# Optimization experiments

Measured on AMD Instinct MI355X. Metric: run time of the kernel, lower is better.

The kernel has to match this reference:

```python
import jax, jax.numpy as jnp
import numpy as np

B, S, D = 2, 2048, 1024
H = 16
HD = D // H  # head_dim = 64


def setup_inputs() -> dict:
    key = jax.random.key(0)
    ks = jax.random.split(key, 9)
    std = 1.0 / np.sqrt(HD)
    inp = {
        "X": jax.random.normal(ks[0], (B, S, D), dtype=jnp.float32),
        # per-head Q/K/V Linear weights stacked: [H, head_dim, head_dim], biases [H, head_dim]
        "Wq": jax.random.uniform(ks[1], (H, HD, HD), jnp.float32, -std, std),
        "bq": jax.random.uniform(ks[2], (H, HD), jnp.float32, -std, std),
        "Wk": jax.random.uniform(ks[3], (H, HD, HD), jnp.float32, -std, std),
        "bk": jax.random.uniform(ks[4], (H, HD), jnp.float32, -std, std),
        "Wv": jax.random.uniform(ks[5], (H, HD, HD), jnp.float32, -std, std),
        "bv": jax.random.uniform(ks[6], (H, HD), jnp.float32, -std, std),
        # output projection: [D, D] (in, out layout), bias [D]
        "Wo": jax.random.uniform(ks[7], (D, D), jnp.float32, -1.0 / np.sqrt(D), 1.0 / np.sqrt(D)),
        "bo": jax.random.uniform(ks[8], (D,), jnp.float32, -1.0 / np.sqrt(D), 1.0 / np.sqrt(D)),
    }
    return inp


def reference(X, Wq, bq, Wk, bk, Wv, bv, Wo, bo):
    # Split hidden dim into heads: [B, S, H, HD]
    x = X.reshape(B, S, H, HD)
    scale = jnp.sqrt(jnp.asarray(HD, dtype=X.dtype))
    # Per-head linear projections (batched over heads)
    Q = jnp.einsum("bshd,hde->bshe", x, Wq) + bq
    K = jnp.einsum("bshd,hde->bshe", x, Wk) + bk
    V = jnp.einsum("bshd,hde->bshe", x, Wv) + bv
    # Attention scores [B, H, S, S]
    scores = jnp.einsum("bshd,bthd->bhst", Q, K) / scale
    attn = jax.nn.softmax(scores, axis=-1)
    # Weighted values -> [B, S, H, HD] -> concat -> [B, S, D]
    out = jnp.einsum("bhst,bthd->bshd", attn, V).reshape(B, S, D)
    return out @ Wo + bo
```

## Files before the change

### kernel.cpp

```cpp
#include <hip/hip_runtime.h>
#include <stdint.h>

#define B_  2
#define S_  2048
#define D_  1024
#define H_  16
#define HD_ 64
#define TOK (B_*S_)

typedef __bf16 bf16x8 __attribute__((ext_vector_type(8)));
typedef __bf16 bf16x4 __attribute__((ext_vector_type(4)));
typedef float  f32x4  __attribute__((ext_vector_type(4)));

static_assert(sizeof(bf16x8) == 16, "bf16x8 must be 16B");
static_assert(sizeof(bf16x4) == 8,  "bf16x4 must be 8B");

__device__ __forceinline__ float fexp2(float x) { return __builtin_amdgcn_exp2f(x); }

__device__ __forceinline__ f32x4 mfma16(bf16x8 a, bf16x8 b, f32x4 c) {
    return __builtin_amdgcn_mfma_f32_16x16x32_bf16(a, b, c, 0, 0, 0);
}

__global__ __launch_bounds__(256) void k_transpose_wo(
    const float* __restrict__ Wo, unsigned short* __restrict__ WoT)
{
    __shared__ float t[64][65];
    const int i0 = blockIdx.x * 64;
    const int o0 = blockIdx.y * 64;
    const int tid = threadIdx.x;
    #pragma unroll
    for (int p = 0; p < 16; ++p) {
        int idx = tid + p * 256;
        int r = idx >> 6, c = idx & 63;
        t[r][c] = Wo[(size_t)(i0 + r) * D_ + o0 + c];
    }
    __syncthreads();
    #pragma unroll
    for (int p = 0; p < 16; ++p) {
        int idx = tid + p * 256;
        int r = idx >> 6, c = idx & 63;
        reinterpret_cast<__bf16*>(WoT)[(size_t)(o0 + r) * D_ + i0 + c] = (__bf16)t[c][r];
    }
}

__global__ __launch_bounds__(256) void k_qkv(
    const float* __restrict__ X,
    const float* __restrict__ Wq, const float* __restrict__ bq,
    const float* __restrict__ Wk, const float* __restrict__ bk,
    const float* __restrict__ Wv, const float* __restrict__ bv,
    unsigned short* __restrict__ Qo, unsigned short* __restrict__ Ko,
    unsigned short* __restrict__ Vt)
{
    __shared__ float          Wf[64][65];
    __shared__ unsigned short Xl[128 * 64];
    __shared__ unsigned short Wl[64 * 64];

    const int tid  = threadIdx.x;
    const int lane = tid & 63, w = tid >> 6;
    const int g = lane >> 4, q = lane & 15;
    const int tok0 = blockIdx.x * 128;
    const int h    = blockIdx.y;
    const int z    = blockIdx.z;
    const float* W  = (z == 0) ? Wq : (z == 1) ? Wk : Wv;
    const float* bb = (z == 0) ? bq : (z == 1) ? bk : bv;

    #pragma unroll
    for (int i = 0; i < 4; ++i) {
        int c = tid + 256 * i;
        int r = c >> 4, c4 = (c & 15) * 4;
        *reinterpret_cast<float4*>(&Wf[r][c4]) =
            *reinterpret_cast<const float4*>(&W[h * 4096 + r * 64 + c4]);
    }
    #pragma unroll
    for (int i = 0; i < 4; ++i) {
        int c = tid + 256 * i;
        int row = c >> 3, slot = c & 7;
        const float* src = &X[(size_t)(tok0 + row) * D_ + h * HD_ + slot * 8];
        float4 x0 = *reinterpret_cast<const float4*>(src);
        float4 x1 = *reinterpret_cast<const float4*>(src + 4);
        bf16x8 v = { (__bf16)x0.x, (__bf16)x0.y, (__bf16)x0.z, (__bf16)x0.w,
                     (__bf16)x1.x, (__bf16)x1.y, (__bf16)x1.z, (__bf16)x1.w };
        *reinterpret_cast<bf16x8*>(
            reinterpret_cast<char*>(Xl) + row * 128 + ((slot ^ (row & 7)) * 16)) = v;
    }
    __syncthreads();

    #pragma unroll
    for (int i = 0; i < 2; ++i) {
        int c = tid + 256 * i;
        int e = c >> 3, slot = c & 7;
        bf16x8 v;
        #pragma unroll
        for (int j = 0; j < 8; ++j) v[j] = (__bf16)Wf[slot * 8 + j][e];
        *reinterpret_cast<bf16x8*>(
            reinterpret_cast<char*>(Wl) + e * 128 + ((slot ^ (e & 7)) * 16)) = v;
    }
    __syncthreads();

    f32x4 acc[2][4] = {};
    #pragma unroll
    for (int s = 0; s < 2; ++s) {
        bf16x8 af[2], bfr[4];
        #pragma unroll
        for (int am = 0; am < 2; ++am) {
            int row  = w * 32 + am * 16 + q;
            int slot = (s * 4 + g) ^ (row & 7);
            af[am] = *reinterpret_cast<const bf16x8*>(
                reinterpret_cast<const char*>(Xl) + row * 128 + slot * 16);
        }
        #pragma unroll
        for (int bn = 0; bn < 4; ++bn) {
            int row  = bn * 16 + q;
            int slot = (s * 4 + g) ^ (row & 7);
            bfr[bn] = *reinterpret_cast<const bf16x8*>(
                reinterpret_cast<const char*>(Wl) + row * 128 + slot * 16);
        }
        #pragma unroll
        for (int am = 0; am < 2; ++am)
            #pragma unroll
            for (int bn = 0; bn < 4; ++bn)
                acc[am][bn] = mfma16(af[am], bfr[bn], acc[am][bn]);
    }

    const float scq = 0.18033688011112042f;
    const int b  = tok0 >> 11;
    const int sb = (tok0 & (S_ - 1)) + w * 32;
    #pragma unroll
    for (int bn = 0; bn < 4; ++bn) {
        int e = bn * 16 + q;
        float bia = bb[h * HD_ + e];
        #pragma unroll
        for (int am = 0; am < 2; ++am) {
            int s4 = sb + am * 16 + 4 * g;
            if (z == 2) {
                bf16x4 ov = { (__bf16)(acc[am][bn][0] + bia), (__bf16)(acc[am][bn][1] + bia),
                              (__bf16)(acc[am][bn][2] + bia), (__bf16)(acc[am][bn][3] + bia) };
                *reinterpret_cast<bf16x4*>(
                    &Vt[((size_t)(b * H_ + h) * HD_ + e) * S_ + s4]) = ov;
            } else {
                float sc = (z == 0) ? scq : 1.0f;
                unsigned short* dst = (z == 0) ? Qo : Ko;
                __bf16* d16 = reinterpret_cast<__bf16*>(dst);
                #pragma unroll
                for (int j = 0; j < 4; ++j)
                    d16[((size_t)(b * H_ + h) * S_ + s4 + j) * HD_ + e] =
                        (__bf16)((acc[am][bn][j] + bia) * sc);
            }
        }
    }
}

__global__ __launch_bounds__(256) void k_attn(
    const unsigned short* __restrict__ Q,
    const unsigned short* __restrict__ K,
    const unsigned short* __restrict__ V,
    unsigned short* __restrict__ O)
{
    __shared__ unsigned short K_lds[2][32 * 72];
    __shared__ unsigned short V_lds[2][64 * 40];
    __shared__ unsigned short P_lds[4][16 * 40];

    const int bh = blockIdx.y;
    const unsigned short* Qp = Q + (size_t)bh * S_ * HD_;
    const unsigned short* Kp = K + (size_t)bh * S_ * HD_;
    const unsigned short* Vp = V + (size_t)bh * HD_ * S_;

    const int tid  = threadIdx.x;
    const int lane = tid & 63, w = tid >> 6;
    const int g = lane >> 4, q = lane & 15;
    const int q0 = blockIdx.x * 64 + w * 16;

    bf16x8 qf0 = *reinterpret_cast<const bf16x8*>(&Qp[(size_t)(q0 + q) * HD_ + 8 * g]);
    bf16x8 qf1 = *reinterpret_cast<const bf16x8*>(&Qp[(size_t)(q0 + q) * HD_ + 32 + 8 * g]);

    f32x4 acc0 = {0.f, 0.f, 0.f, 0.f}, acc1 = acc0, acc2 = acc0, acc3 = acc0;
    float m = -3.0e38f, lp = 0.0f;

    const int kr = tid >> 3, ks = (tid & 7) * 8;
    const int vr = tid >> 2, vs = (tid & 3) * 8;
    unsigned short* Pw = P_lds[w];

    const unsigned short* kSrc = Kp + (size_t)kr * HD_ + ks;
    const unsigned short* vSrc = Vp + (size_t)vr * S_  + vs;

    {
        uint4 k0 = *reinterpret_cast<const uint4*>(kSrc);
        uint4 v0 = *reinterpret_cast<const uint4*>(vSrc);
        *reinterpret_cast<uint4*>(&K_lds[0][kr * 72 + ks]) = k0;
        *reinterpret_cast<uint4*>(&V_lds[0][vr * 40 + vs]) = v0;
    }
    __syncthreads();

    const int NT = S_ / 32;
    for (int t = 0; t < NT; ++t) {
        const int cur = t & 1, nxt = cur ^ 1;

        uint4 kn, vn;
        const bool more = (t + 1 < NT);
        if (more) {
            kn = *reinterpret_cast<const uint4*>(kSrc + (size_t)(t + 1) * 32 * HD_);
            vn = *reinterpret_cast<const uint4*>(vSrc + (size_t)(t + 1) * 32);
        }

        const unsigned short* Kb = K_lds[cur];
        const unsigned short* Vb = V_lds[cur];
        bf16x8 k00 = *reinterpret_cast<const bf16x8*>(&Kb[q * 72 + 8 * g]);
        bf16x8 k01 = *reinterpret_cast<const bf16x8*>(&Kb[q * 72 + 32 + 8 * g]);
        bf16x8 k10 = *reinterpret_cast<const bf16x8*>(&Kb[(16 + q) * 72 + 8 * g]);
        bf16x8 k11 = *reinterpret_cast<const bf16x8*>(&Kb[(16 + q) * 72 + 32 + 8 * g]);
        bf16x8 vf0 = *reinterpret_cast<const bf16x8*>(&Vb[(0 * 16 + q) * 40 + 8 * g]);
        bf16x8 vf1 = *reinterpret_cast<const bf16x8*>(&Vb[(1 * 16 + q) * 40 + 8 * g]);
        bf16x8 vf2 = *reinterpret_cast<const bf16x8*>(&Vb[(2 * 16 + q) * 40 + 8 * g]);
        bf16x8 vf3 = *reinterpret_cast<const bf16x8*>(&Vb[(3 * 16 + q) * 40 + 8 * g]);

        f32x4 z4 = {0.f, 0.f, 0.f, 0.f};
        f32x4 s0 = mfma16(k00, qf0, z4); s0 = mfma16(k01, qf1, s0);
        f32x4 s1 = mfma16(k10, qf0, z4); s1 = mfma16(k11, qf1, s1);

        float pmax = fmaxf(fmaxf(fmaxf(s0[0], s0[1]), fmaxf(s0[2], s0[3])),
                           fmaxf(fmaxf(s1[0], s1[1]), fmaxf(s1[2], s1[3])));
        if (!__all(pmax - m <= 8.0f)) {
            float pm = pmax;
            pm = fmaxf(pm, __shfl_xor(pm, 16));
            pm = fmaxf(pm, __shfl_xor(pm, 32));
            float mn  = fmaxf(m, pm);
            float scl = fexp2(m - mn);
            m = mn;
            lp *= scl;
            acc0 *= scl; acc1 *= scl; acc2 *= scl; acc3 *= scl;
        }
        float p0 = fexp2(s0[0] - m), p1 = fexp2(s0[1] - m);
        float p2 = fexp2(s0[2] - m), p3 = fexp2(s0[3] - m);
        float p4 = fexp2(s1[0] - m), p5 = fexp2(s1[1] - m);
        float p6 = fexp2(s1[2] - m), p7 = fexp2(s1[3] - m);
        lp += ((p0 + p1) + (p2 + p3)) + ((p4 + p5) + (p6 + p7));

        bf16x4 pa = { (__bf16)p0, (__bf16)p1, (__bf16)p2, (__bf16)p3 };
        bf16x4 pb = { (__bf16)p4, (__bf16)p5, (__bf16)p6, (__bf16)p7 };
        *reinterpret_cast<bf16x4*>(&Pw[q * 40 + 4 * g])      = pa;
        *reinterpret_cast<bf16x4*>(&Pw[q * 40 + 16 + 4 * g]) = pb;

        bf16x8 pf = *reinterpret_cast<const bf16x8*>(&Pw[q * 40 + 8 * g]);
        acc0 = mfma16(vf0, pf, acc0);
        acc1 = mfma16(vf1, pf, acc1);
        acc2 = mfma16(vf2, pf, acc2);
        acc3 = mfma16(vf3, pf, acc3);

        if (more) {
            *reinterpret_cast<uint4*>(&K_lds[nxt][kr * 72 + ks]) = kn;
            *reinterpret_cast<uint4*>(&V_lds[nxt][vr * 40 + vs]) = vn;
        }
        __syncthreads();
    }

    lp += __shfl_xor(lp, 16);
    lp += __shfl_xor(lp, 32);
    const float inv = 1.0f / lp;
    const int b = bh >> 4, h = bh & 15;
    size_t row = (size_t)(b * S_ + q0 + q) * D_ + h * HD_ + 4 * g;
    __bf16* Ob = reinterpret_cast<__bf16*>(O);
    bf16x4 o0 = { (__bf16)(acc0[0]*inv), (__bf16)(acc0[1]*inv),
                  (__bf16)(acc0[2]*inv), (__bf16)(acc0[3]*inv) };
    bf16x4 o1 = { (__bf16)(acc1[0]*inv), (__bf16)(acc1[1]*inv),
                  (__bf16)(acc1[2]*inv), (__bf16)(acc1[3]*inv) };
    bf16x4 o2 = { (__bf16)(acc2[0]*inv), (__bf16)(acc2[1]*inv),
                  (__bf16)(acc2[2]*inv), (__bf16)(acc2[3]*inv) };
    bf16x4 o3 = { (__bf16)(acc3[0]*inv), (__bf16)(acc3[1]*inv),
                  (__bf16)(acc3[2]*inv), (__bf16)(acc3[3]*inv) };
    *reinterpret_cast<bf16x4*>(&Ob[row + 0])  = o0;
    *reinterpret_cast<bf16x4*>(&Ob[row + 16]) = o1;
    *reinterpret_cast<bf16x4*>(&Ob[row + 32]) = o2;
    *reinterpret_cast<bf16x4*>(&Ob[row + 48]) = o3;
}

__global__ __launch_bounds__(256) void k_out(
    const unsigned short* __restrict__ A,
    const unsigned short* __restrict__ Wt,
    const float* __restrict__ bo,
    float* __restrict__ C)
{
    __shared__ unsigned short Al[2][128 * 64];
    __shared__ unsigned short Bl[2][128 * 64];

    const int tid  = threadIdx.x;
    const int lane = tid & 63, w = tid >> 6;
    const int g = lane >> 4, q = lane & 15;
    const int wr = w & 1, wc = w >> 1;
    const int m0 = blockIdx.x * 128;
    const int n0 = blockIdx.y * 128;

    int    sbyte[4];
    size_t sgA[4], sgB[4];
    #pragma unroll
    for (int i = 0; i < 4; ++i) {
        int c = tid + 256 * i;
        int row = c >> 3, slot = c & 7;
        sbyte[i] = row * 128 + ((slot ^ (row & 7)) * 16);
        sgA[i] = (size_t)(m0 + row) * D_ + slot * 8;
        sgB[i] = (size_t)(n0 + row) * D_ + slot * 8;
    }

    uint4 ra[4], rb[4];
    #pragma unroll
    for (int i = 0; i < 4; ++i) {
        ra[i] = *reinterpret_cast<const uint4*>(A  + sgA[i]);
        rb[i] = *reinterpret_cast<const uint4*>(Wt + sgB[i]);
    }
    #pragma unroll
    for (int i = 0; i < 4; ++i) {
        *reinterpret_cast<uint4*>(reinterpret_cast<char*>(Al[0]) + sbyte[i]) = ra[i];
        *reinterpret_cast<uint4*>(reinterpret_cast<char*>(Bl[0]) + sbyte[i]) = rb[i];
    }
    __syncthreads();

    f32x4 acc[4][4] = {};
    const int NKT = D_ / 64;
    for (int kt = 0; kt < NKT; ++kt) {
        const int cur = kt & 1, nxt = cur ^ 1;
        const bool more = (kt + 1 < NKT);
        if (more) {
            #pragma unroll
            for (int i = 0; i < 4; ++i) {
                ra[i] = *reinterpret_cast<const uint4*>(A  + sgA[i] + (kt + 1) * 64);
                rb[i] = *reinterpret_cast<const uint4*>(Wt + sgB[i] + (kt + 1) * 64);
            }
        }
        const char* Ab = reinterpret_cast<const char*>(Al[cur]);
        const char* Bb = reinterpret_cast<const char*>(Bl[cur]);
        #pragma unroll
        for (int s = 0; s < 2; ++s) {
            bf16x8 af[4], bfr[4];
            #pragma unroll
            for (int am = 0; am < 4; ++am) {
                int row  = wr * 64 + am * 16 + q;
                int slot = (s * 4 + g) ^ (row & 7);
                af[am] = *reinterpret_cast<const bf16x8*>(Ab + row * 128 + slot * 16);
            }
            #pragma unroll
            for (int bn = 0; bn < 4; ++bn) {
                int row  = wc * 64 + bn * 16 + q;
                int slot = (s * 4 + g) ^ (row & 7);
                bfr[bn] = *reinterpret_cast<const bf16x8*>(Bb + row * 128 + slot * 16);
            }
            #pragma unroll
            for (int am = 0; am < 4; ++am)
                #pragma unroll
                for (int bn = 0; bn < 4; ++bn)
                    acc[am][bn] = mfma16(af[am], bfr[bn], acc[am][bn]);
        }
        if (more) {
            #pragma unroll
            for (int i = 0; i < 4; ++i) {
                *reinterpret_cast<uint4*>(reinterpret_cast<char*>(Al[nxt]) + sbyte[i]) = ra[i];
                *reinterpret_cast<uint4*>(reinterpret_cast<char*>(Bl[nxt]) + sbyte[i]) = rb[i];
            }
        }
        __syncthreads();
    }

    #pragma unroll
    for (int bn = 0; bn < 4; ++bn) {
        int n = n0 + wc * 64 + bn * 16 + q;
        float bia = bo[n];
        #pragma unroll
        for (int am = 0; am < 4; ++am) {
            int mbase = m0 + wr * 64 + am * 16 + 4 * g;
            #pragma unroll
            for (int j = 0; j < 4; ++j)
                C[(size_t)(mbase + j) * D_ + n] = acc[am][bn][j] + bia;
        }
    }
}

extern "C" void kernel_launch(void* const* d_in, const int* in_sizes, int n_in,
                              void* d_out, int out_size, void* d_ws, size_t ws_size,
                              hipStream_t stream)
{
    const float* X  = (const float*)d_in[0];
    const float* Wq = (const float*)d_in[1];
    const float* bq = (const float*)d_in[2];
    const float* Wk = (const float*)d_in[3];
    const float* bk = (const float*)d_in[4];
    const float* Wv = (const float*)d_in[5];
    const float* bv = (const float*)d_in[6];
    const float* Wo = (const float*)d_in[7];
    const float* bo = (const float*)d_in[8];
    float* out = (float*)d_out;

    unsigned short* ws = (unsigned short*)d_ws;
    const size_t QN = (size_t)B_ * H_ * S_ * HD_;
    unsigned short* Qb  = ws;
    unsigned short* Kb  = ws + QN;
    unsigned short* Vtb = ws + 2 * QN;
    unsigned short* Ob  = ws + 3 * QN;
    unsigned short* WoT = ws + 4 * QN;

    k_transpose_wo<<<dim3(16, 16), 256, 0, stream>>>(Wo, WoT);
    k_qkv<<<dim3(TOK / 128, H_, 3), 256, 0, stream>>>(X, Wq, bq, Wk, bk, Wv, bv, Qb, Kb, Vtb);
    k_attn<<<dim3(S_ / 64, B_ * H_), 256, 0, stream>>>(Qb, Kb, Vtb, Ob);
    k_out<<<dim3(TOK / 128, D_ / 128), 256, 0, stream>>>(Ob, WoT, bo, out);
}
```

Before: 180.9 us.

## Pretranspose QKV weights, fuse QKV per block, drop LDS staging in attention, shrink output tiles

A new kernel pre-transposes the Wq/Wk/Wv weights to bf16, so one k_qkv block now computes Q, K and V for its token tile, reusing the staged X tile and writing Q/K with vectorized stores. The attention kernel drops its double-buffered LDS K/V staging and barriers, reads K/V fragments straight from global memory, raises wave priority around MFMAs, and remaps block indices so heads are spread across the grid. The output GEMM tile shrinks from 128x128 to 64x64 to launch more blocks. The trade-offs are more global and L2 traffic in attention and less data reuse per block in the output GEMM.

```diff
diff --git a/kernel.cpp b/kernel.cpp
--- a/kernel.cpp
+++ b/kernel.cpp
@@ -43,34 +43,49 @@
     }
 }
 
+__global__ __launch_bounds__(256) void k_transpose_w(
+    const float* __restrict__ Wq, const float* __restrict__ Wk,
+    const float* __restrict__ Wv, unsigned short* __restrict__ WT)
+{
+    __shared__ float t[64][65];
+    const int h = blockIdx.x, z = blockIdx.y;
+    const float* W = (z == 0) ? Wq : (z == 1) ? Wk : Wv;
+    const int tid = threadIdx.x;
+    #pragma unroll
+    for (int p = 0; p < 4; ++p) {
+        int idx = tid + p * 256;
+        int r = idx >> 4, c4 = (idx & 15) * 4;
+        *reinterpret_cast<float4*>(&t[r][c4]) =
+            *reinterpret_cast<const float4*>(&W[h * 4096 + r * 64 + c4]);
+    }
+    __syncthreads();
+    const int e = tid >> 2, db = (tid & 3) * 16;
+    __bf16* out = reinterpret_cast<__bf16*>(WT) + ((size_t)(z * H_ + h) * 64 + e) * 64 + db;
+    #pragma unroll
+    for (int jj = 0; jj < 2; ++jj) {
+        bf16x8 v;
+        #pragma unroll
+        for (int j = 0; j < 8; ++j) v[j] = (__bf16)t[db + jj * 8 + j][e];
+        *reinterpret_cast<bf16x8*>(out + jj * 8) = v;
+    }
+}
+
 __global__ __launch_bounds__(256) void k_qkv(
-    const float* __restrict__ X,
-    const float* __restrict__ Wq, const float* __restrict__ bq,
-    const float* __restrict__ Wk, const float* __restrict__ bk,
-    const float* __restrict__ Wv, const float* __restrict__ bv,
+    const float* __restrict__ X, const unsigned short* __restrict__ WT,
+    const float* __restrict__ bq, const float* __restrict__ bk,
+    const float* __restrict__ bv,
     unsigned short* __restrict__ Qo, unsigned short* __restrict__ Ko,
     unsigned short* __restrict__ Vt)
 {
-    __shared__ float          Wf[64][65];
     __shared__ unsigned short Xl[128 * 64];
-    __shared__ unsigned short Wl[64 * 64];
+    __shared__ unsigned short Wl[3][64 * 64];
 
     const int tid  = threadIdx.x;
     const int lane = tid & 63, w = tid >> 6;
     const int g = lane >> 4, q = lane & 15;
     const int tok0 = blockIdx.x * 128;
     const int h    = blockIdx.y;
-    const int z    = blockIdx.z;
-    const float* W  = (z == 0) ? Wq : (z == 1) ? Wk : Wv;
-    const float* bb = (z == 0) ? bq : (z == 1) ? bk : bv;
-
-    #pragma unroll
-    for (int i = 0; i < 4; ++i) {
-        int c = tid + 256 * i;
-        int r = c >> 4, c4 = (c & 15) * 4;
-        *reinterpret_cast<float4*>(&Wf[r][c4]) =
-            *reinterpret_cast<const float4*>(&W[h * 4096 + r * 64 + c4]);
-    }
+
     #pragma unroll
     for (int i = 0; i < 4; ++i) {
         int c = tid + 256 * i;
@@ -83,68 +98,89 @@
         *reinterpret_cast<bf16x8*>(
             reinterpret_cast<char*>(Xl) + row * 128 + ((slot ^ (row & 7)) * 16)) = v;
     }
+    #pragma unroll
+    for (int zz = 0; zz < 3; ++zz) {
+        #pragma unroll
+        for (int i = 0; i < 2; ++i) {
+            int c = tid + 256 * i;
+            int e = c >> 3, slot = c & 7;
+            bf16x8 v = *reinterpret_cast<const bf16x8*>(
+                &WT[((size_t)(zz * H_ + h) * 64 + e) * 64 + slot * 8]);
+            *reinterpret_cast<bf16x8*>(
+                reinterpret_cast<char*>(Wl[zz]) + e * 128 + ((slot ^ (e & 7)) * 16)) = v;
+        }
+    }
     __syncthreads();
-
-    #pragma unroll
-    for (int i = 0; i < 2; ++i) {
-        int c = tid + 256 * i;
-        int e = c >> 3, slot = c & 7;
-        bf16x8 v;
-        #pragma unroll
-        for (int j = 0; j < 8; ++j) v[j] = (__bf16)Wf[slot * 8 + j][e];
-        *reinterpret_cast<bf16x8*>(
-            reinterpret_cast<char*>(Wl) + e * 128 + ((slot ^ (e & 7)) * 16)) = v;
-    }
-    __syncthreads();
-
-    f32x4 acc[2][4] = {};
-    #pragma unroll
-    for (int s = 0; s < 2; ++s) {
-        bf16x8 af[2], bfr[4];
-        #pragma unroll
-        for (int am = 0; am < 2; ++am) {
-            int row  = w * 32 + am * 16 + q;
-            int slot = (s * 4 + g) ^ (row & 7);
-            af[am] = *reinterpret_cast<const bf16x8*>(
-                reinterpret_cast<const char*>(Xl) + row * 128 + slot * 16);
-        }
-        #pragma unroll
-        for (int bn = 0; bn < 4; ++bn) {
-            int row  = bn * 16 + q;
-            int slot = (s * 4 + g) ^ (row & 7);
-            bfr[bn] = *reinterpret_cast<const bf16x8*>(
-                reinterpret_cast<const char*>(Wl) + row * 128 + slot * 16);
-        }
-        #pragma unroll
-        for (int am = 0; am < 2; ++am)
-            #pragma unroll
-            for (int bn = 0; bn < 4; ++bn)
-                acc[am][bn] = mfma16(af[am], bfr[bn], acc[am][bn]);
-    }
 
     const float scq = 0.18033688011112042f;
     const int b  = tok0 >> 11;
     const int sb = (tok0 & (S_ - 1)) + w * 32;
-    #pragma unroll
-    for (int bn = 0; bn < 4; ++bn) {
-        int e = bn * 16 + q;
-        float bia = bb[h * HD_ + e];
+
+    #pragma unroll
+    for (int z = 0; z < 3; ++z) {
+        const float* bb = (z == 0) ? bq : (z == 1) ? bk : bv;
+        f32x4 acc[2][4] = {};
         #pragma unroll
-        for (int am = 0; am < 2; ++am) {
-            int s4 = sb + am * 16 + 4 * g;
+        for (int s = 0; s < 2; ++s) {
+            bf16x8 af[2], bfr[4];
+            #pragma unroll
+            for (int am = 0; am < 2; ++am) {
+                int row  = w * 32 + am * 16 + q;
+                int slot = (s * 4 + g) ^ (row & 7);
+                af[am] = *reinterpret_cast<const bf16x8*>(
+                    reinterpret_cast<const char*>(Xl) + row * 128 + slot * 16);
+            }
+            #pragma unroll
+            for (int bn = 0; bn < 4; ++bn) {
+                int row  = bn * 16 + q;
+                int slot = (s * 4 + g) ^ (row & 7);
+                bfr[bn] = *reinterpret_cast<const bf16x8*>(
+                    reinterpret_cast<const char*>(Wl[z]) + row * 128 + slot * 16);
+            }
             if (z == 2) {
-                bf16x4 ov = { (__bf16)(acc[am][bn][0] + bia), (__bf16)(acc[am][bn][1] + bia),
-                              (__bf16)(acc[am][bn][2] + bia), (__bf16)(acc[am][bn][3] + bia) };
-                *reinterpret_cast<bf16x4*>(
-                    &Vt[((size_t)(b * H_ + h) * HD_ + e) * S_ + s4]) = ov;
+                #pragma unroll
+                for (int am = 0; am < 2; ++am)
+                    #pragma unroll
+                    for (int bn = 0; bn < 4; ++bn)
+                        acc[am][bn] = mfma16(af[am], bfr[bn], acc[am][bn]);
             } else {
-                float sc = (z == 0) ? scq : 1.0f;
-                unsigned short* dst = (z == 0) ? Qo : Ko;
-                __bf16* d16 = reinterpret_cast<__bf16*>(dst);
                 #pragma unroll
-                for (int j = 0; j < 4; ++j)
-                    d16[((size_t)(b * H_ + h) * S_ + s4 + j) * HD_ + e] =
-                        (__bf16)((acc[am][bn][j] + bia) * sc);
+                for (int am = 0; am < 2; ++am)
+                    #pragma unroll
+                    for (int bn = 0; bn < 4; ++bn)
+                        acc[am][bn] = mfma16(bfr[bn], af[am], acc[am][bn]);
+            }
+        }
+        if (z == 2) {
+            #pragma unroll
+            for (int bn = 0; bn < 4; ++bn) {
+                int e = bn * 16 + q;
+                float bia = bb[h * HD_ + e];
+                #pragma unroll
+                for (int am = 0; am < 2; ++am) {
+                    int s4 = sb + am * 16 + 4 * g;
+                    bf16x4 ov = { (__bf16)(acc[am][bn][0] + bia), (__bf16)(acc[am][bn][1] + bia),
+                                  (__bf16)(acc[am][bn][2] + bia), (__bf16)(acc[am][bn][3] + bia) };
+                    *reinterpret_cast<bf16x4*>(
+                        &Vt[((size_t)(b * H_ + h) * HD_ + e) * S_ + s4]) = ov;
+                }
+            }
+        } else {
+            const float sc = (z == 0) ? scq : 1.0f;
+            unsigned short* dst = (z == 0) ? Qo : Ko;
+            #pragma unroll
+            for (int bn = 0; bn < 4; ++bn) {
+                float4 bia4 = *reinterpret_cast<const float4*>(&bb[h * HD_ + bn * 16 + 4 * g]);
+                #pragma unroll
+                for (int am = 0; am < 2; ++am) {
+                    int tok = sb + am * 16 + q;
+                    bf16x4 ov = { (__bf16)((acc[am][bn][0] + bia4.x) * sc),
+                                  (__bf16)((acc[am][bn][1] + bia4.y) * sc),
+                                  (__bf16)((acc[am][bn][2] + bia4.z) * sc),
+                                  (__bf16)((acc[am][bn][3] + bia4.w) * sc) };
+                    *reinterpret_cast<bf16x4*>(
+                        &dst[((size_t)(b * H_ + h) * S_ + tok) * HD_ + bn * 16 + 4 * g]) = ov;
+                }
             }
         }
     }
@@ -156,11 +192,12 @@
     const unsigned short* __restrict__ V,
     unsigned short* __restrict__ O)
 {
-    __shared__ unsigned short K_lds[2][32 * 72];
-    __shared__ unsigned short V_lds[2][64 * 40];
     __shared__ unsigned short P_lds[4][16 * 40];
 
-    const int bh = blockIdx.y;
+    const int L  = blockIdx.x + (int)gridDim.x * blockIdx.y;
+    const int bh = (L & 7) * 4 + ((L >> 3) & 3);
+    const int sb = L >> 5;
+
     const unsigned short* Qp = Q + (size_t)bh * S_ * HD_;
     const unsigned short* Kp = K + (size_t)bh * S_ * HD_;
     const unsigned short* Vp = V + (size_t)bh * HD_ * S_;
@@ -168,54 +205,36 @@
     const int tid  = threadIdx.x;
     const int lane = tid & 63, w = tid >> 6;
     const int g = lane >> 4, q = lane & 15;
-    const int q0 = blockIdx.x * 64 + w * 16;
+    const int q0 = sb * 64 + w * 16;
 
     bf16x8 qf0 = *reinterpret_cast<const bf16x8*>(&Qp[(size_t)(q0 + q) * HD_ + 8 * g]);
     bf16x8 qf1 = *reinterpret_cast<const bf16x8*>(&Qp[(size_t)(q0 + q) * HD_ + 32 + 8 * g]);
 
     f32x4 acc0 = {0.f, 0.f, 0.f, 0.f}, acc1 = acc0, acc2 = acc0, acc3 = acc0;
     float m = -3.0e38f, lp = 0.0f;
-
-    const int kr = tid >> 3, ks = (tid & 7) * 8;
-    const int vr = tid >> 2, vs = (tid & 3) * 8;
     unsigned short* Pw = P_lds[w];
 
-    const unsigned short* kSrc = Kp + (size_t)kr * HD_ + ks;
-    const unsigned short* vSrc = Vp + (size_t)vr * S_  + vs;
-
-    {
-        uint4 k0 = *reinterpret_cast<const uint4*>(kSrc);
-        uint4 v0 = *reinterpret_cast<const uint4*>(vSrc);
-        *reinterpret_cast<uint4*>(&K_lds[0][kr * 72 + ks]) = k0;
-        *reinterpret_cast<uint4*>(&V_lds[0][vr * 40 + vs]) = v0;
-    }
-    __syncthreads();
-
-    const int NT = S_ / 32;
-    for (int t = 0; t < NT; ++t) {
-        const int cur = t & 1, nxt = cur ^ 1;
-
-        uint4 kn, vn;
-        const bool more = (t + 1 < NT);
-        if (more) {
-            kn = *reinterpret_cast<const uint4*>(kSrc + (size_t)(t + 1) * 32 * HD_);
-            vn = *reinterpret_cast<const uint4*>(vSrc + (size_t)(t + 1) * 32);
-        }
-
-        const unsigned short* Kb = K_lds[cur];
-        const unsigned short* Vb = V_lds[cur];
-        bf16x8 k00 = *reinterpret_cast<const bf16x8*>(&Kb[q * 72 + 8 * g]);
-        bf16x8 k01 = *reinterpret_cast<const bf16x8*>(&Kb[q * 72 + 32 + 8 * g]);
-        bf16x8 k10 = *reinterpret_cast<const bf16x8*>(&Kb[(16 + q) * 72 + 8 * g]);
-        bf16x8 k11 = *reinterpret_cast<const bf16x8*>(&Kb[(16 + q) * 72 + 32 + 8 * g]);
-        bf16x8 vf0 = *reinterpret_cast<const bf16x8*>(&Vb[(0 * 16 + q) * 40 + 8 * g]);
-        bf16x8 vf1 = *reinterpret_cast<const bf16x8*>(&Vb[(1 * 16 + q) * 40 + 8 * g]);
-        bf16x8 vf2 = *reinterpret_cast<const bf16x8*>(&Vb[(2 * 16 + q) * 40 + 8 * g]);
-        bf16x8 vf3 = *reinterpret_cast<const bf16x8*>(&Vb[(3 * 16 + q) * 40 + 8 * g]);
+    const unsigned short* kRow0 = Kp + (size_t)q * HD_ + 8 * g;
+    const unsigned short* kRow1 = Kp + (size_t)(16 + q) * HD_ + 8 * g;
+    const unsigned short* vRow  = Vp + (size_t)q * S_ + 8 * g;
+
+    for (int kv = 0; kv < S_; kv += 32) {
+        const unsigned short* k0p = kRow0 + (size_t)kv * HD_;
+        const unsigned short* k1p = kRow1 + (size_t)kv * HD_;
+        bf16x8 k00 = *reinterpret_cast<const bf16x8*>(k0p);
+        bf16x8 k01 = *reinterpret_cast<const bf16x8*>(k0p + 32);
+        bf16x8 k10 = *reinterpret_cast<const bf16x8*>(k1p);
+        bf16x8 k11 = *reinterpret_cast<const bf16x8*>(k1p + 32);
+        bf16x8 vf0 = *reinterpret_cast<const bf16x8*>(vRow + kv);
+        bf16x8 vf1 = *reinterpret_cast<const bf16x8*>(vRow + 16 * S_ + kv);
+        bf16x8 vf2 = *reinterpret_cast<const bf16x8*>(vRow + 32 * S_ + kv);
+        bf16x8 vf3 = *reinterpret_cast<const bf16x8*>(vRow + 48 * S_ + kv);
 
         f32x4 z4 = {0.f, 0.f, 0.f, 0.f};
+        __builtin_amdgcn_s_setprio(1);
         f32x4 s0 = mfma16(k00, qf0, z4); s0 = mfma16(k01, qf1, s0);
         f32x4 s1 = mfma16(k10, qf0, z4); s1 = mfma16(k11, qf1, s1);
+        __builtin_amdgcn_s_setprio(0);
 
         float pmax = fmaxf(fmaxf(fmaxf(s0[0], s0[1]), fmaxf(s0[2], s0[3])),
                            fmaxf(fmaxf(s1[0], s1[1]), fmaxf(s1[2], s1[3])));
@@ -239,26 +258,22 @@
         bf16x4 pb = { (__bf16)p4, (__bf16)p5, (__bf16)p6, (__bf16)p7 };
         *reinterpret_cast<bf16x4*>(&Pw[q * 40 + 4 * g])      = pa;
         *reinterpret_cast<bf16x4*>(&Pw[q * 40 + 16 + 4 * g]) = pb;
-
         bf16x8 pf = *reinterpret_cast<const bf16x8*>(&Pw[q * 40 + 8 * g]);
+
+        __builtin_amdgcn_s_setprio(1);
         acc0 = mfma16(vf0, pf, acc0);
         acc1 = mfma16(vf1, pf, acc1);
         acc2 = mfma16(vf2, pf, acc2);
         acc3 = mfma16(vf3, pf, acc3);
-
-        if (more) {
-            *reinterpret_cast<uint4*>(&K_lds[nxt][kr * 72 + ks]) = kn;
-            *reinterpret_cast<uint4*>(&V_lds[nxt][vr * 40 + vs]) = vn;
-        }
-        __syncthreads();
+        __builtin_amdgcn_s_setprio(0);
     }
 
     lp += __shfl_xor(lp, 16);
     lp += __shfl_xor(lp, 32);
     const float inv = 1.0f / lp;
     const int b = bh >> 4, h = bh & 15;
+    __bf16* Ob = reinterpret_cast<__bf16*>(O);
     size_t row = (size_t)(b * S_ + q0 + q) * D_ + h * HD_ + 4 * g;
-    __bf16* Ob = reinterpret_cast<__bf16*>(O);
     bf16x4 o0 = { (__bf16)(acc0[0]*inv), (__bf16)(acc0[1]*inv),
                   (__bf16)(acc0[2]*inv), (__bf16)(acc0[3]*inv) };
     bf16x4 o1 = { (__bf16)(acc1[0]*inv), (__bf16)(acc1[1]*inv),
@@ -279,20 +294,20 @@
     const float* __restrict__ bo,
     float* __restrict__ C)
 {
-    __shared__ unsigned short Al[2][128 * 64];
-    __shared__ unsigned short Bl[2][128 * 64];
+    __shared__ unsigned short Al[2][64 * 64];
+    __shared__ unsigned short Bl[2][64 * 64];
 
     const int tid  = threadIdx.x;
     const int lane = tid & 63, w = tid >> 6;
     const int g = lane >> 4, q = lane & 15;
     const int wr = w & 1, wc = w >> 1;
-    const int m0 = blockIdx.x * 128;
-    const int n0 = blockIdx.y * 128;
-
-    int    sbyte[4];
-    size_t sgA[4], sgB[4];
-    #pragma unroll
-    for (int i = 0; i < 4; ++i) {
+    const int m0 = blockIdx.x * 64;
+    const int n0 = blockIdx.y * 64;
+
+    int    sbyte[2];
+    size_t sgA[2], sgB[2];
+    #pragma unroll
+    for (int i = 0; i < 2; ++i) {
         int c = tid + 256 * i;
         int row = c >> 3, slot = c & 7;
         sbyte[i] = row * 128 + ((slot ^ (row & 7)) * 16);
@@ -300,27 +315,27 @@
         sgB[i] = (size_t)(n0 + row) * D_ + slot * 8;
     }
 
-    uint4 ra[4], rb[4];
-    #pragma unroll
-    for (int i = 0; i < 4; ++i) {
+    uint4 ra[2], rb[2];
+    #pragma unroll
+    for (int i = 0; i < 2; ++i) {
         ra[i] = *reinterpret_cast<const uint4*>(A  + sgA[i]);
         rb[i] = *reinterpret_cast<const uint4*>(Wt + sgB[i]);
     }
     #pragma unroll
-    for (int i = 0; i < 4; ++i) {
+    for (int i = 0; i < 2; ++i) {
         *reinterpret_cast<uint4*>(reinterpret_cast<char*>(Al[0]) + sbyte[i]) = ra[i];
         *reinterpret_cast<uint4*>(reinterpret_cast<char*>(Bl[0]) + sbyte[i]) = rb[i];
     }
     __syncthreads();
 
-    f32x4 acc[4][4] = {};
+    f32x4 acc[2][2] = {};
     const int NKT = D_ / 64;
     for (int kt = 0; kt < NKT; ++kt) {
         const int cur = kt & 1, nxt = cur ^ 1;
         const bool more = (kt + 1 < NKT);
         if (more) {
             #pragma unroll
-            for (int i = 0; i < 4; ++i) {
+            for (int i = 0; i < 2; ++i) {
                 ra[i] = *reinterpret_cast<const uint4*>(A  + sgA[i] + (kt + 1) * 64);
                 rb[i] = *reinterpret_cast<const uint4*>(Wt + sgB[i] + (kt + 1) * 64);
             }
@@ -329,28 +344,28 @@
         const char* Bb = reinterpret_cast<const char*>(Bl[cur]);
         #pragma unroll
         for (int s = 0; s < 2; ++s) {
-            bf16x8 af[4], bfr[4];
-            #pragma unroll
-            for (int am = 0; am < 4; ++am) {
-                int row  = wr * 64 + am * 16 + q;
+            bf16x8 af[2], bfr[2];
+            #pragma unroll
+            for (int am = 0; am < 2; ++am) {
+                int row  = wr * 32 + am * 16 + q;
                 int slot = (s * 4 + g) ^ (row & 7);
                 af[am] = *reinterpret_cast<const bf16x8*>(Ab + row * 128 + slot * 16);
             }
             #pragma unroll
-            for (int bn = 0; bn < 4; ++bn) {
-                int row  = wc * 64 + bn * 16 + q;
+            for (int bn = 0; bn < 2; ++bn) {
+                int row  = wc * 32 + bn * 16 + q;
                 int slot = (s * 4 + g) ^ (row & 7);
                 bfr[bn] = *reinterpret_cast<const bf16x8*>(Bb + row * 128 + slot * 16);
             }
             #pragma unroll
-            for (int am = 0; am < 4; ++am)
+            for (int am = 0; am < 2; ++am)
                 #pragma unroll
-                for (int bn = 0; bn < 4; ++bn)
+                for (int bn = 0; bn < 2; ++bn)
                     acc[am][bn] = mfma16(af[am], bfr[bn], acc[am][bn]);
         }
         if (more) {
             #pragma unroll
-            for (int i = 0; i < 4; ++i) {
+            for (int i = 0; i < 2; ++i) {
                 *reinterpret_cast<uint4*>(reinterpret_cast<char*>(Al[nxt]) + sbyte[i]) = ra[i];
                 *reinterpret_cast<uint4*>(reinterpret_cast<char*>(Bl[nxt]) + sbyte[i]) = rb[i];
             }
@@ -359,12 +374,12 @@
     }
 
     #pragma unroll
-    for (int bn = 0; bn < 4; ++bn) {
-        int n = n0 + wc * 64 + bn * 16 + q;
+    for (int bn = 0; bn < 2; ++bn) {
+        int n = n0 + wc * 32 + bn * 16 + q;
         float bia = bo[n];
         #pragma unroll
-        for (int am = 0; am < 4; ++am) {
-            int mbase = m0 + wr * 64 + am * 16 + 4 * g;
+        for (int am = 0; am < 2; ++am) {
+            int mbase = m0 + wr * 32 + am * 16 + 4 * g;
             #pragma unroll
             for (int j = 0; j < 4; ++j)
                 C[(size_t)(mbase + j) * D_ + n] = acc[am][bn][j] + bia;
@@ -389,14 +404,16 @@
 
     unsigned short* ws = (unsigned short*)d_ws;
     const size_t QN = (size_t)B_ * H_ * S_ * HD_;
-    unsigned short* Qb  = ws;
-    unsigned short* Kb  = ws + QN;
-    unsigned short* Vtb = ws + 2 * QN;
-    unsigned short* Ob  = ws + 3 * QN;
-    unsigned short* WoT = ws + 4 * QN;
+    unsigned short* Qb    = ws;
+    unsigned short* Kb    = ws + QN;
+    unsigned short* Vtb   = ws + 2 * QN;
+    unsigned short* Ob    = ws + 3 * QN;
+    unsigned short* WoT   = ws + 4 * QN;
+    unsigned short* WqkvT = ws + 4 * QN + (size_t)D_ * D_;
 
     k_transpose_wo<<<dim3(16, 16), 256, 0, stream>>>(Wo, WoT);
-    k_qkv<<<dim3(TOK / 128, H_, 3), 256, 0, stream>>>(X, Wq, bq, Wk, bk, Wv, bv, Qb, Kb, Vtb);
-    k_attn<<<dim3(S_ / 64, B_ * H_), 256, 0, stream>>>(Qb, Kb, Vtb, Ob);
-    k_out<<<dim3(TOK / 128, D_ / 128), 256, 0, stream>>>(Ob, WoT, bo, out);
-}
+    k_transpose_w<<<dim3(H_, 3), 256, 0, stream>>>(Wq, Wk, Wv, WqkvT);
+    k_qkv<<<dim3(TOK / 128, H_), 256, 0, stream>>>(X, WqkvT, bq, bk, bv, Qb, Kb, Vtb);
+    k_attn<<<dim3(32, 32), 256, 0, stream>>>(Qb, Kb, Vtb, Ob);
+    k_out<<<dim3(TOK / 64, D_ / 64), 256, 0, stream>>>(Ob, WoT, bo, out);
+}
```

After: 338.7 us. +87.2%, slower.
